# Performance work log

Hardware: AMD Instinct MI355X
Metric: run time of the kernel (lower is better)

Reference implementation:

```python
import jax, jax.numpy as jnp
import numpy as np

IN_DIM = 2048
OUT_DIM = 2048
BATCH = 4096

def _xavier(key, fan_in, fan_out):
    std = np.sqrt(2.0 / (fan_in + fan_out)).astype(np.float32)
    return jax.random.normal(key, (fan_in, fan_out), dtype=jnp.float32) * std

def setup_inputs() -> dict:
    key = jax.random.key(0)
    ks = jax.random.split(key, 12)
    inp = {
        'X': jax.random.normal(ks[0], (BATCH, IN_DIM), dtype=jnp.float32),
        'C': jax.random.normal(ks[1], (BATCH, OUT_DIM), dtype=jnp.float32),
        'H': jax.random.normal(ks[2], (BATCH, OUT_DIM), dtype=jnp.float32),
        'W_xf': _xavier(ks[3], IN_DIM, OUT_DIM),
        'W_xg': _xavier(ks[4], IN_DIM, OUT_DIM),
        'W_xi': _xavier(ks[5], IN_DIM, OUT_DIM),
        'W_xo': _xavier(ks[6], IN_DIM, OUT_DIM),
        'W_hf': _xavier(ks[7], OUT_DIM, OUT_DIM),
        'W_hg': _xavier(ks[8], OUT_DIM, OUT_DIM),
        'W_hi': _xavier(ks[9], OUT_DIM, OUT_DIM),
        'W_ho': _xavier(ks[10], OUT_DIM, OUT_DIM),
        'b_f': jnp.zeros((1, OUT_DIM), dtype=jnp.float32),
        'b_g': jnp.zeros((1, OUT_DIM), dtype=jnp.float32),
        'b_i': jnp.zeros((1, OUT_DIM), dtype=jnp.float32),
        'b_o': jnp.zeros((1, OUT_DIM), dtype=jnp.float32),
    }
    return inp

def reference(X, C, H, W_xf, W_xg, W_xi, W_xo, W_hf, W_hg, W_hi, W_ho, b_f, b_g, b_i, b_o):
    # LSTM cell: 4 gates, each x@W_x* + b_* + h@W_h*
    F = jax.nn.sigmoid(X @ W_xf + b_f + H @ W_hf)
    I = jax.nn.sigmoid(X @ W_xi + b_i + H @ W_hi)
    O = jax.nn.sigmoid(X @ W_xo + b_o + H @ W_ho)
    G = jnp.tanh(X @ W_xg + b_g + H @ W_hg)
    C_new = G * I + F * C
    Y = O * jnp.tanh(C_new)
    return (C_new, Y)
```

## Files before the change

### kernel.cpp

```cpp
#include <hip/hip_runtime.h>
#include <cstdint>
#include <cstddef>

#define BATCH   4096
#define IN_DIM  2048
#define OUT_DIM 2048
#define KDIM    4096

typedef __bf16 bf16x8 __attribute__((ext_vector_type(8)));
typedef float  floatx4 __attribute__((ext_vector_type(4)));

__device__ __forceinline__ unsigned short f2bf(float f) {
  unsigned int u = __float_as_uint(f);
  u += 0x7FFFu + ((u >> 16) & 1u);
  return (unsigned short)(u >> 16);
}

__device__ __forceinline__ void async16(const void* g, void* l) {
  __builtin_amdgcn_global_load_lds(
      (const __attribute__((address_space(1))) unsigned int*)g,
      (__attribute__((address_space(3))) unsigned int*)l, 16, 0, 0);
}

__global__ __launch_bounds__(256) void pack_A_kernel(
    const float* __restrict__ X, const float* __restrict__ H,
    unsigned short* __restrict__ A) {
  int idx = blockIdx.x * 256 + threadIdx.x;
  int e = idx << 2;
  int m = e >> 12;
  int k = e & 4095;
  const float* src = (k < IN_DIM) ? (X + (size_t)m * IN_DIM + k)
                                  : (H + (size_t)m * OUT_DIM + (k - IN_DIM));
  float4 v = *(const float4*)src;
  ushort4 o;
  o.x = f2bf(v.x); o.y = f2bf(v.y); o.z = f2bf(v.z); o.w = f2bf(v.w);
  *(ushort4*)(A + e) = o;
}

__global__ __launch_bounds__(256) void pack_B_kernel(
    const float* __restrict__ Wxf, const float* __restrict__ Wxi,
    const float* __restrict__ Wxo, const float* __restrict__ Wxg,
    const float* __restrict__ Whf, const float* __restrict__ Whi,
    const float* __restrict__ Who, const float* __restrict__ Whg,
    unsigned short* __restrict__ Bt) {
  __shared__ float tile[32][33];
  int bx = blockIdx.x;
  int nT = bx >> 7;
  int kT = bx & 127;
  int n0 = nT * 32, k0 = kT * 32;
  int g = n0 >> 11;
  int c0 = n0 & 2047;
  const float* W;
  int kk0;
  if (k0 < IN_DIM) {
    kk0 = k0;
    W = (g == 0) ? Wxf : (g == 1) ? Wxi : (g == 2) ? Wxo : Wxg;
  } else {
    kk0 = k0 - IN_DIM;
    W = (g == 0) ? Whf : (g == 1) ? Whi : (g == 2) ? Who : Whg;
  }
  int t = threadIdx.x;
#pragma unroll
  for (int i = 0; i < 4; ++i) {
    int idx = i * 256 + t;
    int lk = idx >> 5, ln = idx & 31;
    tile[lk][ln] = W[(size_t)(kk0 + lk) * 2048 + c0 + ln];
  }
  __syncthreads();
#pragma unroll
  for (int i = 0; i < 4; ++i) {
    int idx = i * 256 + t;
    int ln = idx >> 5, lk = idx & 31;
    Bt[(size_t)(n0 + ln) * KDIM + k0 + lk] = f2bf(tile[lk][ln]);
  }
}

__global__ __launch_bounds__(256) void lstm_gemm_fused(
    const unsigned short* __restrict__ A,
    const unsigned short* __restrict__ Bt,
    const float* __restrict__ Cin,
    const float* __restrict__ bF, const float* __restrict__ bI,
    const float* __restrict__ bO, const float* __restrict__ bG,
    float* __restrict__ outC, float* __restrict__ outY) {
  __shared__ unsigned short lA[128 * 32];
  __shared__ unsigned short lB[128 * 32];

  const int t = threadIdx.x;
  const int lane = t & 63;
  const int w = t >> 6;
  const int wm = w & 1, wn = w >> 1;
  const int mBase = blockIdx.y * 128;
  const int nBase = blockIdx.x * 32;

  floatx4 acc[4][4];
#pragma unroll
  for (int g = 0; g < 4; ++g)
#pragma unroll
    for (int mt = 0; mt < 4; ++mt) acc[g][mt] = (floatx4){0.f, 0.f, 0.f, 0.f};

  const int rowA = t >> 2;
  const int cb = (t & 3) * 16;
  const char* aG0 = (const char*)(A + (size_t)(mBase + rowA) * KDIM) + cb;
  const char* aG1 = aG0 + (size_t)64 * KDIM * 2;
  const int r1 = 64 + rowA;
  const char* bG0 = (const char*)(Bt + (size_t)((rowA >> 5) * 2048 + nBase + (rowA & 31)) * KDIM) + cb;
  const char* bG1 = (const char*)(Bt + (size_t)((r1 >> 5) * 2048 + nBase + (r1 & 31)) * KDIM) + cb;
  char* lAdst = (char*)lA + t * 16;
  char* lBdst = (char*)lB + t * 16;

  const int fr = lane & 15;
  const int fk = lane >> 4;

  for (int k0 = 0; k0 < KDIM; k0 += 32) {
    const int kb = k0 * 2;
    async16(aG0 + kb, lAdst);
    async16(aG1 + kb, lAdst + 4096);
    async16(bG0 + kb, lBdst);
    async16(bG1 + kb, lBdst + 4096);
    __syncthreads();

    const bf16x8* A8 = (const bf16x8*)lA;
    const bf16x8* B8 = (const bf16x8*)lB;
    bf16x8 af[4], bf[4];
#pragma unroll
    for (int mt = 0; mt < 4; ++mt) af[mt] = A8[(wm * 64 + mt * 16 + fr) * 4 + fk];
#pragma unroll
    for (int g = 0; g < 4; ++g)   bf[g] = B8[(g * 32 + wn * 16 + fr) * 4 + fk];
#pragma unroll
    for (int g = 0; g < 4; ++g)
#pragma unroll
      for (int mt = 0; mt < 4; ++mt)
        acc[g][mt] = __builtin_amdgcn_mfma_f32_16x16x32_bf16(af[mt], bf[g], acc[g][mt], 0, 0, 0);
    __syncthreads();
  }

  const int col = nBase + wn * 16 + (lane & 15);
  const int rbase = mBase + wm * 64 + (lane >> 4) * 4;
  const float bfv = bF[col], biv = bI[col], bov = bO[col], bgv = bG[col];
#pragma unroll
  for (int mt = 0; mt < 4; ++mt) {
#pragma unroll
    for (int r = 0; r < 4; ++r) {
      const int row = rbase + mt * 16 + r;
      const size_t off = (size_t)row * OUT_DIM + col;
      float pf = acc[0][mt][r] + bfv;
      float pi = acc[1][mt][r] + biv;
      float po = acc[2][mt][r] + bov;
      float pg = acc[3][mt][r] + bgv;
      float F = 1.f / (1.f + __expf(-pf));
      float I = 1.f / (1.f + __expf(-pi));
      float O = 1.f / (1.f + __expf(-po));
      float G = tanhf(pg);
      float c_new = G * I + F * Cin[off];
      outC[off] = c_new;
      outY[off] = O * tanhf(c_new);
    }
  }
}

extern "C" void kernel_launch(void* const* d_in, const int* in_sizes, int n_in,
                              void* d_out, int out_size, void* d_ws, size_t ws_size,
                              hipStream_t stream) {
  const float* X   = (const float*)d_in[0];
  const float* C   = (const float*)d_in[1];
  const float* H   = (const float*)d_in[2];
  const float* Wxf = (const float*)d_in[3];
  const float* Wxg = (const float*)d_in[4];
  const float* Wxi = (const float*)d_in[5];
  const float* Wxo = (const float*)d_in[6];
  const float* Whf = (const float*)d_in[7];
  const float* Whg = (const float*)d_in[8];
  const float* Whi = (const float*)d_in[9];
  const float* Who = (const float*)d_in[10];
  const float* bf_ = (const float*)d_in[11];
  const float* bg_ = (const float*)d_in[12];
  const float* bi_ = (const float*)d_in[13];
  const float* bo_ = (const float*)d_in[14];

  float* outC = (float*)d_out;
  float* outY = (float*)d_out + (size_t)BATCH * OUT_DIM;

  unsigned short* A  = (unsigned short*)d_ws;
  unsigned short* Bt = A + (size_t)BATCH * KDIM;

  pack_A_kernel<<<(BATCH * KDIM / 4) / 256, 256, 0, stream>>>(X, H, A);
  pack_B_kernel<<<256 * 128, 256, 0, stream>>>(Wxf, Wxi, Wxo, Wxg,
                                               Whf, Whi, Who, Whg, Bt);
  dim3 grid(OUT_DIM / 32, BATCH / 128);
  lstm_gemm_fused<<<grid, 256, 0, stream>>>(A, Bt, C, bf_, bi_, bo_, bg_,
                                            outC, outY);
}
```

Before: 609.4 us.

## Enlarge GEMM M-tile, swizzle LDS, vectorize weight packing, use fast tanh

The fused LSTM GEMM block tile grows from 128 to 256 rows, with each wave owning 64 rows and both 16-column N fragments per gate. This doubles reuse of B fragments and halves the grid height. An XOR swizzle is added to the LDS column layout to cut bank conflicts on fragment reads. The weight pack kernel now uses float4 loads and 16-byte packed bf16 stores, tanhf is replaced by an exp-based approximation, and launch bounds request 2 blocks per SIMD. Register pressure rises with 32 accumulators per thread, which may limit occupancy.

Result: faster. 531.2 us (-12.8%).

```diff
diff --git a/kernel.cpp b/kernel.cpp
--- a/kernel.cpp
+++ b/kernel.cpp
@@ -20,6 +20,10 @@
   __builtin_amdgcn_global_load_lds(
       (const __attribute__((address_space(1))) unsigned int*)g,
       (__attribute__((address_space(3))) unsigned int*)l, 16, 0, 0);
+}
+
+__device__ __forceinline__ float tanh_fast(float x) {
+  return 1.f - 2.f / (__expf(2.f * x) + 1.f);
 }
 
 __global__ __launch_bounds__(256) void pack_A_kernel(
@@ -43,11 +47,11 @@
     const float* __restrict__ Whf, const float* __restrict__ Whi,
     const float* __restrict__ Who, const float* __restrict__ Whg,
     unsigned short* __restrict__ Bt) {
-  __shared__ float tile[32][33];
+  __shared__ float tile[64][33];
   int bx = blockIdx.x;
-  int nT = bx >> 7;
-  int kT = bx & 127;
-  int n0 = nT * 32, k0 = kT * 32;
+  int kT = bx & 63;
+  int nT = bx >> 6;
+  int k0 = kT * 64, n0 = nT * 32;
   int g = n0 >> 11;
   int c0 = n0 & 2047;
   const float* W;
@@ -61,99 +65,122 @@
   }
   int t = threadIdx.x;
 #pragma unroll
-  for (int i = 0; i < 4; ++i) {
+  for (int i = 0; i < 2; ++i) {
     int idx = i * 256 + t;
-    int lk = idx >> 5, ln = idx & 31;
-    tile[lk][ln] = W[(size_t)(kk0 + lk) * 2048 + c0 + ln];
+    int lk = idx >> 3, lc = (idx & 7) * 4;
+    float4 v = *(const float4*)(W + (size_t)(kk0 + lk) * 2048 + c0 + lc);
+    tile[lk][lc]     = v.x;
+    tile[lk][lc + 1] = v.y;
+    tile[lk][lc + 2] = v.z;
+    tile[lk][lc + 3] = v.w;
   }
   __syncthreads();
-#pragma unroll
-  for (int i = 0; i < 4; ++i) {
-    int idx = i * 256 + t;
-    int ln = idx >> 5, lk = idx & 31;
-    Bt[(size_t)(n0 + ln) * KDIM + k0 + lk] = f2bf(tile[lk][ln]);
-  }
-}
-
-__global__ __launch_bounds__(256) void lstm_gemm_fused(
+  int ln = t >> 3, k8 = (t & 7) * 8;
+  unsigned int p[4];
+#pragma unroll
+  for (int j = 0; j < 4; ++j) {
+    unsigned int lo = f2bf(tile[k8 + 2 * j][ln]);
+    unsigned int hi = f2bf(tile[k8 + 2 * j + 1][ln]);
+    p[j] = lo | (hi << 16);
+  }
+  uint4 o = make_uint4(p[0], p[1], p[2], p[3]);
+  *(uint4*)(Bt + (size_t)(n0 + ln) * KDIM + k0 + k8) = o;
+}
+
+__global__ __launch_bounds__(256, 2) void lstm_gemm_fused(
     const unsigned short* __restrict__ A,
     const unsigned short* __restrict__ Bt,
     const float* __restrict__ Cin,
     const float* __restrict__ bF, const float* __restrict__ bI,
     const float* __restrict__ bO, const float* __restrict__ bG,
     float* __restrict__ outC, float* __restrict__ outY) {
-  __shared__ unsigned short lA[128 * 32];
+  __shared__ unsigned short lA[256 * 32];
   __shared__ unsigned short lB[128 * 32];
 
   const int t = threadIdx.x;
   const int lane = t & 63;
   const int w = t >> 6;
-  const int wm = w & 1, wn = w >> 1;
-  const int mBase = blockIdx.y * 128;
+  const int mBase = blockIdx.y * 256;
   const int nBase = blockIdx.x * 32;
 
-  floatx4 acc[4][4];
+  floatx4 acc[4][2][4];
 #pragma unroll
   for (int g = 0; g < 4; ++g)
 #pragma unroll
-    for (int mt = 0; mt < 4; ++mt) acc[g][mt] = (floatx4){0.f, 0.f, 0.f, 0.f};
-
-  const int rowA = t >> 2;
-  const int cb = (t & 3) * 16;
-  const char* aG0 = (const char*)(A + (size_t)(mBase + rowA) * KDIM) + cb;
-  const char* aG1 = aG0 + (size_t)64 * KDIM * 2;
-  const int r1 = 64 + rowA;
-  const char* bG0 = (const char*)(Bt + (size_t)((rowA >> 5) * 2048 + nBase + (rowA & 31)) * KDIM) + cb;
-  const char* bG1 = (const char*)(Bt + (size_t)((r1 >> 5) * 2048 + nBase + (r1 & 31)) * KDIM) + cb;
+    for (int nf = 0; nf < 2; ++nf)
+#pragma unroll
+      for (int mt = 0; mt < 4; ++mt) acc[g][nf][mt] = (floatx4){0.f, 0.f, 0.f, 0.f};
+
+  const int rowT = t >> 2;
+  const int cswz = (((t & 3) ^ ((t >> 3) & 3))) * 16;
+  const char* aG = (const char*)(A + (size_t)(mBase + rowT) * KDIM) + cswz;
+  const size_t aStep = (size_t)64 * KDIM * 2;
+  const int r1 = 64 + rowT;
+  const char* bG0 = (const char*)(Bt + (size_t)((rowT >> 5) * 2048 + nBase + (rowT & 31)) * KDIM) + cswz;
+  const char* bG1 = (const char*)(Bt + (size_t)((r1 >> 5) * 2048 + nBase + (r1 & 31)) * KDIM) + cswz;
   char* lAdst = (char*)lA + t * 16;
   char* lBdst = (char*)lB + t * 16;
 
   const int fr = lane & 15;
   const int fk = lane >> 4;
+  const int fkx = fk ^ ((fr >> 1) & 3);
 
   for (int k0 = 0; k0 < KDIM; k0 += 32) {
     const int kb = k0 * 2;
-    async16(aG0 + kb, lAdst);
-    async16(aG1 + kb, lAdst + 4096);
-    async16(bG0 + kb, lBdst);
-    async16(bG1 + kb, lBdst + 4096);
+    async16(aG + kb,             lAdst);
+    async16(aG + kb + aStep,     lAdst + 4096);
+    async16(aG + kb + 2 * aStep, lAdst + 8192);
+    async16(aG + kb + 3 * aStep, lAdst + 12288);
+    async16(bG0 + kb,            lBdst);
+    async16(bG1 + kb,            lBdst + 4096);
     __syncthreads();
 
     const bf16x8* A8 = (const bf16x8*)lA;
     const bf16x8* B8 = (const bf16x8*)lB;
-    bf16x8 af[4], bf[4];
-#pragma unroll
-    for (int mt = 0; mt < 4; ++mt) af[mt] = A8[(wm * 64 + mt * 16 + fr) * 4 + fk];
-#pragma unroll
-    for (int g = 0; g < 4; ++g)   bf[g] = B8[(g * 32 + wn * 16 + fr) * 4 + fk];
+    bf16x8 af[4], bfrag[8];
+#pragma unroll
+    for (int mt = 0; mt < 4; ++mt)
+      af[mt] = A8[(w * 64 + mt * 16 + fr) * 4 + fkx];
 #pragma unroll
     for (int g = 0; g < 4; ++g)
 #pragma unroll
-      for (int mt = 0; mt < 4; ++mt)
-        acc[g][mt] = __builtin_amdgcn_mfma_f32_16x16x32_bf16(af[mt], bf[g], acc[g][mt], 0, 0, 0);
+      for (int nf = 0; nf < 2; ++nf)
+        bfrag[g * 2 + nf] = B8[(g * 32 + nf * 16 + fr) * 4 + fkx];
+#pragma unroll
+    for (int g = 0; g < 4; ++g)
+#pragma unroll
+      for (int nf = 0; nf < 2; ++nf)
+#pragma unroll
+        for (int mt = 0; mt < 4; ++mt)
+          acc[g][nf][mt] = __builtin_amdgcn_mfma_f32_16x16x32_bf16(
+              af[mt], bfrag[g * 2 + nf], acc[g][nf][mt], 0, 0, 0);
     __syncthreads();
   }
 
-  const int col = nBase + wn * 16 + (lane & 15);
-  const int rbase = mBase + wm * 64 + (lane >> 4) * 4;
-  const float bfv = bF[col], biv = bI[col], bov = bO[col], bgv = bG[col];
-#pragma unroll
-  for (int mt = 0; mt < 4; ++mt) {
-#pragma unroll
-    for (int r = 0; r < 4; ++r) {
-      const int row = rbase + mt * 16 + r;
-      const size_t off = (size_t)row * OUT_DIM + col;
-      float pf = acc[0][mt][r] + bfv;
-      float pi = acc[1][mt][r] + biv;
-      float po = acc[2][mt][r] + bov;
-      float pg = acc[3][mt][r] + bgv;
-      float F = 1.f / (1.f + __expf(-pf));
-      float I = 1.f / (1.f + __expf(-pi));
-      float O = 1.f / (1.f + __expf(-po));
-      float G = tanhf(pg);
-      float c_new = G * I + F * Cin[off];
-      outC[off] = c_new;
-      outY[off] = O * tanhf(c_new);
+  const int col0 = nBase + (lane & 15);
+  const int rb = mBase + w * 64 + (lane >> 4) * 4;
+#pragma unroll
+  for (int nf = 0; nf < 2; ++nf) {
+    const int col = col0 + nf * 16;
+    const float bfv = bF[col], biv = bI[col], bov = bO[col], bgv = bG[col];
+#pragma unroll
+    for (int mt = 0; mt < 4; ++mt) {
+#pragma unroll
+      for (int r = 0; r < 4; ++r) {
+        const int row = rb + mt * 16 + r;
+        const size_t off = (size_t)row * OUT_DIM + col;
+        float pf = acc[0][nf][mt][r] + bfv;
+        float pi = acc[1][nf][mt][r] + biv;
+        float po = acc[2][nf][mt][r] + bov;
+        float pg = acc[3][nf][mt][r] + bgv;
+        float F = 1.f / (1.f + __expf(-pf));
+        float I = 1.f / (1.f + __expf(-pi));
+        float O = 1.f / (1.f + __expf(-po));
+        float G = tanh_fast(pg);
+        float c_new = G * I + F * Cin[off];
+        outC[off] = c_new;
+        outY[off] = O * tanh_fast(c_new);
+      }
     }
   }
 }
@@ -184,9 +211,9 @@
   unsigned short* Bt = A + (size_t)BATCH * KDIM;
 
   pack_A_kernel<<<(BATCH * KDIM / 4) / 256, 256, 0, stream>>>(X, H, A);
-  pack_B_kernel<<<256 * 128, 256, 0, stream>>>(Wxf, Wxi, Wxo, Wxg,
-                                               Whf, Whi, Who, Whg, Bt);
-  dim3 grid(OUT_DIM / 32, BATCH / 128);
+  pack_B_kernel<<<64 * 256, 256, 0, stream>>>(Wxf, Wxi, Wxo, Wxg,
+                                              Whf, Whi, Who, Whg, Bt);
+  dim3 grid(OUT_DIM / 32, BATCH / 256);
   lstm_gemm_fused<<<grid, 256, 0, stream>>>(A, Bt, C, bf_, bi_, bo_, bg_,
                                             outC, outY);
 }
```
